# Optimization experiments

Measured on AMD Instinct MI355X. Metric: run time of the kernel, lower is better.

The kernel has to match this reference:

```python
import jax, jax.numpy as jnp
import numpy as np

B, S, E = 2, 2048, 1024
H, KV, D = 16, 4, 64
GC = 128          # ve_gate_channels
EPS = 1.1920929e-07  # torch F.rms_norm default eps for fp32
NEG = -1e30


def setup_inputs() -> dict:
    key = jax.random.key(0)
    ks = jax.random.split(key, 8)
    x = jax.random.normal(ks[0], (B, S, E), jnp.float32)
    ve = jax.random.normal(ks[1], (B, S, KV * D), jnp.float32)
    half = D // 2
    inv_freq = 1.0 / (10000.0 ** (np.arange(half, dtype=np.float64) / half))
    ang = np.arange(S, dtype=np.float64)[:, None] * inv_freq[None, :]
    cos = jnp.asarray(np.cos(ang), jnp.float32)[:, None, :]  # [S,1,D/2]
    sin = jnp.asarray(np.sin(ang), jnp.float32)[:, None, :]
    sc = E ** -0.5
    Wq = jax.random.normal(ks[2], (E, H * D), jnp.float32) * sc
    Wk = jax.random.normal(ks[3], (E, KV * D), jnp.float32) * sc
    Wv = jax.random.normal(ks[4], (E, KV * D), jnp.float32) * sc
    Wproj = jax.random.normal(ks[5], (E, E), jnp.float32) * sc
    Wgate = jax.random.normal(ks[6], (GC, KV), jnp.float32) * (GC ** -0.5)
    return {"x": x, "ve": ve, "cos": cos, "sin": sin, "Wq": Wq, "Wk": Wk,
            "Wv": Wv, "Wproj": Wproj, "Wgate": Wgate,
            "window_left": 1024, "window_right": 0}


def _rms(x):
    return x * jax.lax.rsqrt(jnp.mean(x * x, axis=-1, keepdims=True) + EPS)


def _rope(x, cos, sin):
    d = x.shape[-1] // 2
    x1, x2 = x[..., :d], x[..., d:]
    return jnp.concatenate([x1 * cos + x2 * sin, -x1 * sin + x2 * cos], axis=-1)


def reference(x, ve, cos, sin, Wq, Wk, Wv, Wproj, Wgate, window_left, window_right):
    b, s, e = x.shape
    q = (x @ Wq).reshape(b, s, H, D)
    k = (x @ Wk).reshape(b, s, KV, D)
    v = (x @ Wv).reshape(b, s, KV, D)
    # value-embedding gate: 2*sigmoid over first GC channels, per kv-head
    gate = 2.0 * jax.nn.sigmoid(x[..., :GC] @ Wgate)          # [B,S,KV]
    v = v + gate[..., None] * ve.reshape(b, s, KV, D)
    q = _rms(_rope(q, cos, sin))
    k = _rms(_rope(k, cos, sin))
    # GQA: repeat kv heads to match query heads
    g = H // KV
    kk = jnp.repeat(k, g, axis=2)                             # [B,S,H,D]
    vv = jnp.repeat(v, g, axis=2)
    scores = jnp.einsum('bihd,bjhd->bhij', q, kk) * (D ** -0.5)
    i = jnp.arange(s)[:, None]
    j = jnp.arange(s)[None, :]
    mask = (j <= i + window_right) & (j >= i - window_left) & (j <= i)
    scores = jnp.where(mask, scores, NEG)
    p = jax.nn.softmax(scores, axis=-1)
    y = jnp.einsum('bhij,bjhd->bihd', p, vv).reshape(b, s, H * D)
    return y @ Wproj
```

## Files before the change

### kernel.cpp

```cpp
#include <hip/hip_runtime.h>

typedef __bf16 bf16;
typedef __bf16 bf16x4 __attribute__((ext_vector_type(4)));
typedef __bf16 bf16x8 __attribute__((ext_vector_type(8)));
typedef float floatx4 __attribute__((ext_vector_type(4)));

#define EPS 1.1920929e-07f
#define QSCALE (0.125f * 1.44269504088896f)
#define SHIFT_C 11.5416f

__device__ __forceinline__ floatx4 mfma16(bf16x8 a, bf16x8 b, floatx4 c) {
  return __builtin_amdgcn_mfma_f32_16x16x32_bf16(a, b, c, 0, 0, 0);
}

__device__ __forceinline__ void gload16(const void* g, void* l) {
  __builtin_amdgcn_global_load_lds((const __attribute__((address_space(1))) unsigned int*)g,
                                   (__attribute__((address_space(3))) unsigned int*)l, 16, 0, 0);
}

__global__ void cast_x_kernel(const float* __restrict__ x, bf16* __restrict__ xb) {
  int i = (blockIdx.x * blockDim.x + threadIdx.x) * 4;
  float4 v = *(const float4*)(x + i);
  bf16x4 o = {(bf16)v.x, (bf16)v.y, (bf16)v.z, (bf16)v.w};
  *(bf16x4*)(xb + i) = o;
}

__global__ void pack_wqkv_kernel(const float* __restrict__ Wq, const float* __restrict__ Wk,
                                 const float* __restrict__ Wv, bf16* __restrict__ out) {
  __shared__ float tile[32][33];
  int n0 = blockIdx.x * 32, k0 = blockIdx.y * 32;
  int tx = threadIdx.x & 31, ty = threadIdx.x >> 5;
#pragma unroll
  for (int i = 0; i < 4; i++) {
    int k = k0 + ty + i * 8, n = n0 + tx;
    float v;
    if (n < 1024)      v = Wq[(size_t)k * 1024 + n];
    else if (n < 1280) v = Wk[(size_t)k * 256 + (n - 1024)];
    else               v = Wv[(size_t)k * 256 + (n - 1280)];
    tile[ty + i * 8][tx] = v;
  }
  __syncthreads();
#pragma unroll
  for (int i = 0; i < 4; i++) {
    int n = n0 + ty + i * 8, k = k0 + tx;
    out[(size_t)n * 1024 + k] = (bf16)tile[tx][ty + i * 8];
  }
}

__global__ void trans_wproj_kernel(const float* __restrict__ W, bf16* __restrict__ out) {
  __shared__ float tile[32][33];
  int n0 = blockIdx.x * 32, k0 = blockIdx.y * 32;
  int tx = threadIdx.x & 31, ty = threadIdx.x >> 5;
#pragma unroll
  for (int i = 0; i < 4; i++)
    tile[ty + i * 8][tx] = W[(size_t)(k0 + ty + i * 8) * 1024 + n0 + tx];
  __syncthreads();
#pragma unroll
  for (int i = 0; i < 4; i++)
    out[(size_t)(n0 + ty + i * 8) * 1024 + k0 + tx] = (bf16)tile[tx][ty + i * 8];
}

template <bool OUT_BF16>
__global__ __launch_bounds__(256) void gemm_kernel(const bf16* __restrict__ A,
                                                   const bf16* __restrict__ Bt,
                                                   void* __restrict__ Cout,
                                                   int M, int N, int K) {
  __shared__ bf16 As[128 * 32];
  __shared__ bf16 Bs[64 * 32];
  const int tid = threadIdx.x;
  const int m0 = blockIdx.y * 128, n0 = blockIdx.x * 64;
  const int w = tid >> 6, lane = tid & 63;
  const int q = lane >> 4, r0 = lane & 15;
  const int wm = w & 1, wn = w >> 1;
  const int lrow = lane >> 2, lcol = (lane & 3) * 8;

  floatx4 acc[4][2];
#pragma unroll
  for (int i = 0; i < 4; i++)
#pragma unroll
    for (int j = 0; j < 2; j++) acc[i][j] = (floatx4){0.f, 0.f, 0.f, 0.f};

  for (int k0 = 0; k0 < K; k0 += 32) {
    __syncthreads();
    gload16(A + (size_t)(m0 + w * 16 + lrow) * K + k0 + lcol, &As[(w * 16) * 32]);
    gload16(A + (size_t)(m0 + 64 + w * 16 + lrow) * K + k0 + lcol, &As[(64 + w * 16) * 32]);
    gload16(Bt + (size_t)(n0 + w * 16 + lrow) * K + k0 + lcol, &Bs[(w * 16) * 32]);
    __syncthreads();
    bf16x8 af[4], bfr[2];
#pragma unroll
    for (int mt = 0; mt < 4; mt++) af[mt] = *(const bf16x8*)&As[(wm * 64 + mt * 16 + r0) * 32 + q * 8];
#pragma unroll
    for (int nt = 0; nt < 2; nt++) bfr[nt] = *(const bf16x8*)&Bs[(wn * 32 + nt * 16 + r0) * 32 + q * 8];
#pragma unroll
    for (int mt = 0; mt < 4; mt++)
#pragma unroll
      for (int nt = 0; nt < 2; nt++)
        acc[mt][nt] = mfma16(af[mt], bfr[nt], acc[mt][nt]);
  }
#pragma unroll
  for (int mt = 0; mt < 4; mt++)
#pragma unroll
    for (int nt = 0; nt < 2; nt++)
#pragma unroll
      for (int r = 0; r < 4; r++) {
        int row = m0 + wm * 64 + mt * 16 + q * 4 + r;
        int col = n0 + wn * 32 + nt * 16 + r0;
        float v = acc[mt][nt][r];
        if (OUT_BF16) ((bf16*)Cout)[(size_t)row * N + col] = (bf16)v;
        else          ((float*)Cout)[(size_t)row * N + col] = v;
      }
}

__global__ void postproc_kernel(const bf16* __restrict__ qkv, const float* __restrict__ x,
                                const float* __restrict__ ve, const float* __restrict__ cosb,
                                const float* __restrict__ sinb, const float* __restrict__ wgate,
                                bf16* __restrict__ Qb, bf16* __restrict__ Kb, bf16* __restrict__ Vb) {
  int t = blockIdx.x;
  int b = t >> 11, s = t & 2047;
  int w = threadIdx.x >> 6, lane = threadIdx.x & 63;

  const float* xrow = x + (size_t)t * 1024;
  float g = xrow[lane] * wgate[lane * 4 + w] + xrow[64 + lane] * wgate[(64 + lane) * 4 + w];
  for (int m = 1; m < 64; m <<= 1) g += __shfl_xor(g, m, 64);
  g = 2.f / (1.f + __expf(-g));

  int d = lane & 31;
  float c = cosb[s * 32 + d], sn = sinb[s * 32 + d];
  float sgn = (lane < 32) ? sn : -sn;
  const bf16* qrow = qkv + (size_t)t * 1536;

#pragma unroll
  for (int i = 0; i < 4; i++) {
    int h = w * 4 + i;
    float v = (float)qrow[h * 64 + lane];
    float p = __shfl_xor(v, 32, 64);
    float rv = v * c + p * sgn;
    float ss = rv * rv;
    for (int m = 1; m < 64; m <<= 1) ss += __shfl_xor(ss, m, 64);
    float outq = rv * rsqrtf(ss * (1.f / 64.f) + EPS) * QSCALE;
    Qb[(((size_t)b * 16 + h) * 2048 + s) * 64 + lane] = (bf16)outq;
  }
  {
    float v = (float)qrow[1024 + w * 64 + lane];
    float p = __shfl_xor(v, 32, 64);
    float rv = v * c + p * sgn;
    float ss = rv * rv;
    for (int m = 1; m < 64; m <<= 1) ss += __shfl_xor(ss, m, 64);
    float outk = rv * rsqrtf(ss * (1.f / 64.f) + EPS);
    Kb[(((size_t)b * 4 + w) * 2048 + s) * 64 + lane] = (bf16)outk;
    float vv = (float)qrow[1280 + w * 64 + lane] + g * ve[(size_t)t * 256 + w * 64 + lane];
    Vb[(((size_t)b * 4 + w) * 2048 + s) * 64 + lane] = (bf16)vv;
  }
}

__global__ void pack_kv_kernel(const bf16* __restrict__ Kb, const bf16* __restrict__ Vb,
                               bf16* __restrict__ Kf, bf16* __restrict__ Vf) {
  __shared__ bf16 Ks[64 * 72];
  __shared__ bf16 Vs[64 * 72];
  int chunk = blockIdx.x;
  int bkv = blockIdx.y;
  const bf16* kin = Kb + ((size_t)bkv * 2048 + chunk * 64) * 64;
  const bf16* vin = Vb + ((size_t)bkv * 2048 + chunk * 64) * 64;
  int t = threadIdx.x;
  int row = t >> 3, col = (t & 7) * 8;
#pragma unroll
  for (int i = 0; i < 2; i++) {
    *(uint4*)&Ks[(row + 32 * i) * 72 + col] = *(const uint4*)(kin + (size_t)(row + 32 * i) * 64 + col);
    *(uint4*)&Vs[(row + 32 * i) * 72 + col] = *(const uint4*)(vin + (size_t)(row + 32 * i) * 64 + col);
  }
  __syncthreads();
  int lane = t & 63, q = (t >> 4) & 3, r0 = t & 15;
  int sub = t >> 7;
  int pair = (t >> 6) & 1;
  size_t tbase = ((size_t)bkv * 64 + chunk * 2 + sub) * 2048;
#pragma unroll
  for (int i = 0; i < 2; i++) {
    int w = pair * 2 + i;
    int jl = sub * 32 + (w >= 2 ? 16 : 0) + r0;
    int d0 = (w & 1) * 32 + q * 8;
    *(uint4*)&Kf[tbase + w * 512 + lane * 8] = *(const uint4*)&Ks[jl * 72 + d0];
  }
#pragma unroll
  for (int i = 0; i < 2; i++) {
    int nt = pair * 2 + i;
    int d = nt * 16 + r0;
    bf16 tmp[8];
#pragma unroll
    for (int e = 0; e < 8; e++) {
      int jl = sub * 32 + (e >> 2) * 16 + 4 * q + (e & 3);
      tmp[e] = Vs[jl * 72 + d];
    }
    *(uint4*)&Vf[tbase + nt * 512 + lane * 8] = *(uint4*)tmp;
  }
}

__global__ __launch_bounds__(512, 4) void attn_kernel(const bf16* __restrict__ Qb,
                                                      const bf16* __restrict__ Kf,
                                                      const bf16* __restrict__ Vf,
                                                      const int* __restrict__ wlp,
                                                      const int* __restrict__ wrp,
                                                      bf16* __restrict__ Yb) {
  __shared__ float Ol[4 * 64 * 21];
  const int wl = wlp[0];
  const int wrc = min(wrp[0], 0);
  const int blk = blockIdx.x;
  const int qc = 31 - (blk & 31);
  const int bh = blk >> 5;
  const int b = bh >> 4, h = bh & 15, kvh = (bh & 15) >> 2;
  const int w = threadIdx.x >> 6, lane = threadIdx.x & 63;
  const int wq = w & 3, jh = w >> 2;
  const int q = lane >> 4, r0 = lane & 15;
  const int q0 = qc * 64 + wq * 16;

  const bf16* qbase = Qb + (((size_t)b * 16 + h) * 2048 + q0 + r0) * 64;
  bf16x8 aq0 = *(const bf16x8*)(qbase + q * 8);
  bf16x8 aq1 = *(const bf16x8*)(qbase + 32 + q * 8);

  floatx4 Oacc[4];
#pragma unroll
  for (int nt = 0; nt < 4; nt++) Oacc[nt] = (floatx4){0.f, 0.f, 0.f, 0.f};
  floatx4 Lacc = (floatx4){0.f, 0.f, 0.f, 0.f};

  const bf16 onev = (bf16)1.0f;
  const bf16x8 ones = {onev, onev, onev, onev, onev, onev, onev, onev};

  const int jlo0 = max(0, q0 - wl) & ~31;
  const int jhi = q0 + 15 + wrc;
  const int n = ((jhi - jlo0) >> 5) + 1;
  const int nlo = (n + 1) >> 1;
  const int jstart = jh ? jlo0 + (nlo << 5) : jlo0;
  const int count = jh ? n - nlo : nlo;

  const bf16* kfb = Kf + ((size_t)(b * 4 + kvh) * 64) * 2048 + lane * 8;
  const bf16* vfb = Vf + ((size_t)(b * 4 + kvh) * 64) * 2048 + lane * 8;

  if (count > 0) {
    int tile0 = jstart >> 5;
    bf16x8 kf[4], vf[4], nk[4], nv[4];
#pragma unroll
    for (int u = 0; u < 4; u++) {
      kf[u] = *(const bf16x8*)(kfb + (size_t)tile0 * 2048 + u * 512);
      vf[u] = *(const bf16x8*)(vfb + (size_t)tile0 * 2048 + u * 512);
    }

    for (int t = 0; t < count; t++) {
      const int j0 = jstart + (t << 5);
      const int tn = (t + 1 < count) ? tile0 + t + 1 : tile0 + t;
#pragma unroll
      for (int u = 0; u < 4; u++) {
        nk[u] = *(const bf16x8*)(kfb + (size_t)tn * 2048 + u * 512);
        nv[u] = *(const bf16x8*)(vfb + (size_t)tn * 2048 + u * 512);
      }

      floatx4 s0 = (floatx4){-SHIFT_C, -SHIFT_C, -SHIFT_C, -SHIFT_C};
      floatx4 s1 = s0;
      s0 = mfma16(kf[0], aq0, s0);
      s0 = mfma16(kf[1], aq1, s0);
      s1 = mfma16(kf[2], aq0, s1);
      s1 = mfma16(kf[3], aq1, s1);

      bf16x8 pa;
      if (j0 >= q0 + 15 - wl && j0 + 31 <= q0 + wrc) {
#pragma unroll
        for (int r = 0; r < 4; r++) {
          pa[r] = (bf16)exp2f(s0[r]);
          pa[4 + r] = (bf16)exp2f(s1[r]);
        }
      } else {
        const int i = q0 + r0;
#pragma unroll
        for (int r = 0; r < 4; r++) {
          int ja = j0 + 4 * q + r, jb = ja + 16;
          bool va = (ja <= i + wrc) && (ja >= i - wl);
          bool vb = (jb <= i + wrc) && (jb >= i - wl);
          pa[r] = va ? (bf16)exp2f(s0[r]) : (bf16)0.f;
          pa[4 + r] = vb ? (bf16)exp2f(s1[r]) : (bf16)0.f;
        }
      }

      Lacc = mfma16(pa, ones, Lacc);
#pragma unroll
      for (int nt = 0; nt < 4; nt++) Oacc[nt] = mfma16(pa, vf[nt], Oacc[nt]);

#pragma unroll
      for (int u = 0; u < 4; u++) { kf[u] = nk[u]; vf[u] = nv[u]; }
    }
  }

  float* mbase = Ol + (wq * 64 + lane) * 21;
  if (jh == 1) {
#pragma unroll
    for (int nt = 0; nt < 4; nt++)
#pragma unroll
      for (int r = 0; r < 4; r++) mbase[nt * 4 + r] = Oacc[nt][r];
#pragma unroll
    for (int r = 0; r < 4; r++) mbase[16 + r] = Lacc[r];
  }
  __syncthreads();
  if (jh == 0) {
    float inv[4];
#pragma unroll
    for (int r = 0; r < 4; r++) inv[r] = 1.f / (Lacc[r] + mbase[16 + r]);
#pragma unroll
    for (int nt = 0; nt < 4; nt++)
#pragma unroll
      for (int r = 0; r < 4; r++) {
        int i = q0 + q * 4 + r;
        float o = (Oacc[nt][r] + mbase[nt * 4 + r]) * inv[r];
        Yb[((size_t)b * 2048 + i) * 1024 + h * 64 + nt * 16 + r0] = (bf16)o;
      }
  }
}

extern "C" void kernel_launch(void* const* d_in, const int* in_sizes, int n_in,
                              void* d_out, int out_size, void* d_ws, size_t ws_size,
                              hipStream_t stream) {
  const float* x     = (const float*)d_in[0];
  const float* ve    = (const float*)d_in[1];
  const float* cosb  = (const float*)d_in[2];
  const float* sinb  = (const float*)d_in[3];
  const float* Wq    = (const float*)d_in[4];
  const float* Wk    = (const float*)d_in[5];
  const float* Wv    = (const float*)d_in[6];
  const float* Wproj = (const float*)d_in[7];
  const float* Wgate = (const float*)d_in[8];
  const int* wl      = (const int*)d_in[9];
  const int* wr      = (const int*)d_in[10];

  char* ws = (char*)d_ws;
  bf16* Xb      = (bf16*)(ws);
  bf16* Wqkv_t  = (bf16*)(ws + 8388608);
  bf16* Wproj_t = (bf16*)(ws + 11534336);
  bf16* qkvb    = (bf16*)(ws + 13631488);
  bf16* Qb      = (bf16*)(ws + 26214400);
  bf16* Kb      = (bf16*)(ws + 34603008);
  bf16* Kf      = (bf16*)(ws + 36700160);
  bf16* Yb      = (bf16*)(ws + 38797312);
  bf16* Vb      = Yb;
  bf16* Vf      = qkvb;

  cast_x_kernel<<<4096, 256, 0, stream>>>(x, Xb);
  pack_wqkv_kernel<<<dim3(48, 32), 256, 0, stream>>>(Wq, Wk, Wv, Wqkv_t);
  trans_wproj_kernel<<<dim3(32, 32), 256, 0, stream>>>(Wproj, Wproj_t);
  gemm_kernel<true><<<dim3(24, 32), 256, 0, stream>>>(Xb, Wqkv_t, qkvb, 4096, 1536, 1024);
  postproc_kernel<<<4096, 256, 0, stream>>>(qkvb, x, ve, cosb, sinb, Wgate, Qb, Kb, Vb);
  pack_kv_kernel<<<dim3(32, 8), 256, 0, stream>>>(Kb, Vb, Kf, Vf);
  attn_kernel<<<1024, 512, 0, stream>>>(Qb, Kf, Vf, wl, wr, Yb);
  gemm_kernel<false><<<dim3(16, 32), 256, 0, stream>>>(Yb, Wproj_t, d_out, 4096, 1024, 1024);
}
```

Before: 198.4 us.

## Fuse RoPE, RMS norm, value gate and KV packing into QKV GEMM epilogue

The QKV GEMM now uses 128x128 tiles, and its epilogue does the work of the old postproc and pack kernels. It applies RoPE and RMS norm to Q and K, adds the gated value embedding to V, and writes Q, K and V straight into the attention-ready layouts through LDS staging. This removes the bf16 qkv intermediate round trip and two launches. A small separate kernel computes the sigmoid gate. The output projection GEMM also moves to 128x128 tiles. The trade-off is fewer blocks per GEMM (384 and 256), which may lower occupancy and load balance on a 256-CU device, plus the new serial gate kernel.

```diff
diff --git a/kernel.cpp b/kernel.cpp
--- a/kernel.cpp
+++ b/kernel.cpp
@@ -60,138 +60,240 @@
     out[(size_t)(n0 + ty + i * 8) * 1024 + k0 + tx] = (bf16)tile[tx][ty + i * 8];
 }
 
-template <bool OUT_BF16>
-__global__ __launch_bounds__(256) void gemm_kernel(const bf16* __restrict__ A,
-                                                   const bf16* __restrict__ Bt,
-                                                   void* __restrict__ Cout,
-                                                   int M, int N, int K) {
-  __shared__ bf16 As[128 * 32];
-  __shared__ bf16 Bs[64 * 32];
+__global__ void gate_kernel(const float* __restrict__ x, const float* __restrict__ wgate,
+                            float* __restrict__ gate) {
+  int tid = blockIdx.x * 256 + threadIdx.x;
+  int t = tid >> 2, kv = tid & 3;
+  const float* xr = x + (size_t)t * 1024;
+  float g = 0.f;
+#pragma unroll 4
+  for (int c = 0; c < 128; c++) g += xr[c] * wgate[c * 4 + kv];
+  int b = t >> 11, s = t & 2047;
+  gate[((size_t)b * 4 + kv) * 2048 + s] = 2.f / (1.f + __expf(-g));
+}
+
+__global__ __launch_bounds__(256) void qkv_gemm_kernel(const bf16* __restrict__ A,
+                                                       const bf16* __restrict__ Bt,
+                                                       const float* __restrict__ ve,
+                                                       const float* __restrict__ cosb,
+                                                       const float* __restrict__ sinb,
+                                                       const float* __restrict__ gate,
+                                                       bf16* __restrict__ Qb,
+                                                       bf16* __restrict__ Kf,
+                                                       bf16* __restrict__ Vf) {
+  __shared__ __align__(16) char smem[36864];
+  bf16* As = (bf16*)smem;
+  bf16* Bs = (bf16*)(smem + 8192);
+  bf16* Ep = (bf16*)smem;
+  const int K = 1024;
   const int tid = threadIdx.x;
-  const int m0 = blockIdx.y * 128, n0 = blockIdx.x * 64;
+  const int tile = blockIdx.x;
+  const int m0 = blockIdx.y * 128, n0 = tile * 128;
   const int w = tid >> 6, lane = tid & 63;
   const int q = lane >> 4, r0 = lane & 15;
   const int wm = w & 1, wn = w >> 1;
   const int lrow = lane >> 2, lcol = (lane & 3) * 8;
-
-  floatx4 acc[4][2];
+  const int b = m0 >> 11, s0 = m0 & 2047;
+
+  floatx4 acc[4][4];
 #pragma unroll
   for (int i = 0; i < 4; i++)
 #pragma unroll
-    for (int j = 0; j < 2; j++) acc[i][j] = (floatx4){0.f, 0.f, 0.f, 0.f};
+    for (int j = 0; j < 4; j++) acc[i][j] = (floatx4){0.f, 0.f, 0.f, 0.f};
 
   for (int k0 = 0; k0 < K; k0 += 32) {
     __syncthreads();
-    gload16(A + (size_t)(m0 + w * 16 + lrow) * K + k0 + lcol, &As[(w * 16) * 32]);
-    gload16(A + (size_t)(m0 + 64 + w * 16 + lrow) * K + k0 + lcol, &As[(64 + w * 16) * 32]);
-    gload16(Bt + (size_t)(n0 + w * 16 + lrow) * K + k0 + lcol, &Bs[(w * 16) * 32]);
-    __syncthreads();
-    bf16x8 af[4], bfr[2];
+    gload16(A + (size_t)(m0 + w * 32 + lrow) * K + k0 + lcol, &As[(w * 32) * 32]);
+    gload16(A + (size_t)(m0 + w * 32 + 16 + lrow) * K + k0 + lcol, &As[(w * 32 + 16) * 32]);
+    gload16(Bt + (size_t)(n0 + w * 32 + lrow) * K + k0 + lcol, &Bs[(w * 32) * 32]);
+    gload16(Bt + (size_t)(n0 + w * 32 + 16 + lrow) * K + k0 + lcol, &Bs[(w * 32 + 16) * 32]);
+    __syncthreads();
+    bf16x8 af[4], bfr[4];
 #pragma unroll
     for (int mt = 0; mt < 4; mt++) af[mt] = *(const bf16x8*)&As[(wm * 64 + mt * 16 + r0) * 32 + q * 8];
 #pragma unroll
-    for (int nt = 0; nt < 2; nt++) bfr[nt] = *(const bf16x8*)&Bs[(wn * 32 + nt * 16 + r0) * 32 + q * 8];
+    for (int nt = 0; nt < 4; nt++) bfr[nt] = *(const bf16x8*)&Bs[(wn * 64 + nt * 16 + r0) * 32 + q * 8];
 #pragma unroll
     for (int mt = 0; mt < 4; mt++)
 #pragma unroll
-      for (int nt = 0; nt < 2; nt++)
+      for (int nt = 0; nt < 4; nt++)
         acc[mt][nt] = mfma16(af[mt], bfr[nt], acc[mt][nt]);
   }
+  __syncthreads();
+
+  if (tile < 8) {
+#pragma unroll
+    for (int mt = 0; mt < 4; mt++) {
+      float rvv[4][4];
+#pragma unroll
+      for (int ntp = 0; ntp < 2; ntp++) {
+        int d31 = ntp * 16 + r0;
+#pragma unroll
+        for (int r = 0; r < 4; r++) {
+          int s = s0 + wm * 64 + mt * 16 + q * 4 + r;
+          float c = cosb[s * 32 + d31], sn = sinb[s * 32 + d31];
+          float v1 = acc[mt][ntp][r], v2 = acc[mt][ntp + 2][r];
+          rvv[ntp][r] = v1 * c + v2 * sn;
+          rvv[ntp + 2][r] = v2 * c - v1 * sn;
+        }
+      }
+#pragma unroll
+      for (int r = 0; r < 4; r++) {
+        float ss = 0.f;
+#pragma unroll
+        for (int nt = 0; nt < 4; nt++) ss += rvv[nt][r] * rvv[nt][r];
+        ss += __shfl_xor(ss, 1, 64);
+        ss += __shfl_xor(ss, 2, 64);
+        ss += __shfl_xor(ss, 4, 64);
+        ss += __shfl_xor(ss, 8, 64);
+        float sc = rsqrtf(ss * (1.f / 64.f) + EPS) * QSCALE;
+        int row = wm * 64 + mt * 16 + q * 4 + r;
+#pragma unroll
+        for (int nt = 0; nt < 4; nt++)
+          Ep[(wn * 128 + row) * 72 + nt * 16 + r0] = (bf16)(rvv[nt][r] * sc);
+      }
+    }
+    __syncthreads();
+#pragma unroll
+    for (int p = 0; p < 8; p++) {
+      int g = p * 256 + tid;
+      int plane = g >> 10, rem = g & 1023, row = rem >> 3, chunk = rem & 7;
+      uint4 val = *(const uint4*)&Ep[(plane * 128 + row) * 72 + chunk * 8];
+      int h = tile * 2 + plane;
+      *(uint4*)&Qb[(((size_t)b * 16 + h) * 2048 + s0 + row) * 64 + chunk * 8] = val;
+    }
+  } else if (tile < 10) {
+    int kv = (tile - 8) * 2 + wn;
+#pragma unroll
+    for (int mt = 0; mt < 4; mt++) {
+      float rvv[4][4];
+#pragma unroll
+      for (int ntp = 0; ntp < 2; ntp++) {
+        int d31 = ntp * 16 + r0;
+#pragma unroll
+        for (int r = 0; r < 4; r++) {
+          int s = s0 + wm * 64 + mt * 16 + q * 4 + r;
+          float c = cosb[s * 32 + d31], sn = sinb[s * 32 + d31];
+          float v1 = acc[mt][ntp][r], v2 = acc[mt][ntp + 2][r];
+          rvv[ntp][r] = v1 * c + v2 * sn;
+          rvv[ntp + 2][r] = v2 * c - v1 * sn;
+        }
+      }
+#pragma unroll
+      for (int r = 0; r < 4; r++) {
+        float ss = 0.f;
+#pragma unroll
+        for (int nt = 0; nt < 4; nt++) ss += rvv[nt][r] * rvv[nt][r];
+        ss += __shfl_xor(ss, 1, 64);
+        ss += __shfl_xor(ss, 2, 64);
+        ss += __shfl_xor(ss, 4, 64);
+        ss += __shfl_xor(ss, 8, 64);
+        float sc = rsqrtf(ss * (1.f / 64.f) + EPS);
+        int row = wm * 64 + mt * 16 + q * 4 + r;
+#pragma unroll
+        for (int nt = 0; nt < 4; nt++)
+          Ep[(wn * 128 + row) * 72 + nt * 16 + r0] = (bf16)(rvv[nt][r] * sc);
+      }
+    }
+    __syncthreads();
+#pragma unroll
+    for (int st = 0; st < 2; st++) {
+      int tk = (s0 >> 5) + wm * 2 + st;
+      size_t tb = ((size_t)(b * 4 + kv) * 64 + tk) * 2048;
+#pragma unroll
+      for (int u = 0; u < 4; u++) {
+        int joff = (u >= 2) ? 16 : 0, doff = (u & 1) * 32;
+        bf16x8 f = *(const bf16x8*)&Ep[(wn * 128 + wm * 64 + st * 32 + joff + r0) * 72 + doff + q * 8];
+        *(bf16x8*)&Kf[tb + u * 512 + lane * 8] = f;
+      }
+    }
+  } else {
+    int kv = (tile - 10) * 2 + wn;
+    const float* gbase = gate + ((size_t)b * 4 + kv) * 2048;
+#pragma unroll
+    for (int mt = 0; mt < 4; mt++) {
+#pragma unroll
+      for (int r = 0; r < 4; r++) {
+        int row = wm * 64 + mt * 16 + q * 4 + r;
+        int t = m0 + row;
+        float gg = gbase[s0 + row];
+#pragma unroll
+        for (int nt = 0; nt < 4; nt++) {
+          int d = nt * 16 + r0;
+          float vv = acc[mt][nt][r] + gg * ve[(size_t)t * 256 + kv * 64 + d];
+          Ep[(wn * 128 + row) * 72 + d] = (bf16)vv;
+        }
+      }
+    }
+    __syncthreads();
+#pragma unroll
+    for (int st = 0; st < 2; st++) {
+      int tk = (s0 >> 5) + wm * 2 + st;
+      size_t tb = ((size_t)(b * 4 + kv) * 64 + tk) * 2048;
+#pragma unroll
+      for (int nt = 0; nt < 4; nt++) {
+        bf16 tmp[8];
+#pragma unroll
+        for (int e = 0; e < 8; e++) {
+          int jl = wm * 64 + st * 32 + (e >> 2) * 16 + 4 * q + (e & 3);
+          tmp[e] = Ep[(wn * 128 + jl) * 72 + nt * 16 + r0];
+        }
+        *(uint4*)&Vf[tb + nt * 512 + lane * 8] = *(uint4*)tmp;
+      }
+    }
+  }
+}
+
+template <bool OUT_BF16>
+__global__ __launch_bounds__(256) void gemm128_kernel(const bf16* __restrict__ A,
+                                                      const bf16* __restrict__ Bt,
+                                                      void* __restrict__ Cout,
+                                                      int M, int N, int K) {
+  __shared__ __align__(16) bf16 As[128 * 32];
+  __shared__ __align__(16) bf16 Bs[128 * 32];
+  const int tid = threadIdx.x;
+  const int m0 = blockIdx.y * 128, n0 = blockIdx.x * 128;
+  const int w = tid >> 6, lane = tid & 63;
+  const int q = lane >> 4, r0 = lane & 15;
+  const int wm = w & 1, wn = w >> 1;
+  const int lrow = lane >> 2, lcol = (lane & 3) * 8;
+
+  floatx4 acc[4][4];
+#pragma unroll
+  for (int i = 0; i < 4; i++)
+#pragma unroll
+    for (int j = 0; j < 4; j++) acc[i][j] = (floatx4){0.f, 0.f, 0.f, 0.f};
+
+  for (int k0 = 0; k0 < K; k0 += 32) {
+    __syncthreads();
+    gload16(A + (size_t)(m0 + w * 32 + lrow) * K + k0 + lcol, &As[(w * 32) * 32]);
+    gload16(A + (size_t)(m0 + w * 32 + 16 + lrow) * K + k0 + lcol, &As[(w * 32 + 16) * 32]);
+    gload16(Bt + (size_t)(n0 + w * 32 + lrow) * K + k0 + lcol, &Bs[(w * 32) * 32]);
+    gload16(Bt + (size_t)(n0 + w * 32 + 16 + lrow) * K + k0 + lcol, &Bs[(w * 32 + 16) * 32]);
+    __syncthreads();
+    bf16x8 af[4], bfr[4];
+#pragma unroll
+    for (int mt = 0; mt < 4; mt++) af[mt] = *(const bf16x8*)&As[(wm * 64 + mt * 16 + r0) * 32 + q * 8];
+#pragma unroll
+    for (int nt = 0; nt < 4; nt++) bfr[nt] = *(const bf16x8*)&Bs[(wn * 64 + nt * 16 + r0) * 32 + q * 8];
+#pragma unroll
+    for (int mt = 0; mt < 4; mt++)
+#pragma unroll
+      for (int nt = 0; nt < 4; nt++)
+        acc[mt][nt] = mfma16(af[mt], bfr[nt], acc[mt][nt]);
+  }
 #pragma unroll
   for (int mt = 0; mt < 4; mt++)
 #pragma unroll
-    for (int nt = 0; nt < 2; nt++)
+    for (int nt = 0; nt < 4; nt++)
 #pragma unroll
       for (int r = 0; r < 4; r++) {
         int row = m0 + wm * 64 + mt * 16 + q * 4 + r;
-        int col = n0 + wn * 32 + nt * 16 + r0;
+        int col = n0 + wn * 64 + nt * 16 + r0;
         float v = acc[mt][nt][r];
         if (OUT_BF16) ((bf16*)Cout)[(size_t)row * N + col] = (bf16)v;
         else          ((float*)Cout)[(size_t)row * N + col] = v;
       }
-}
-
-__global__ void postproc_kernel(const bf16* __restrict__ qkv, const float* __restrict__ x,
-                                const float* __restrict__ ve, const float* __restrict__ cosb,
-                                const float* __restrict__ sinb, const float* __restrict__ wgate,
-                                bf16* __restrict__ Qb, bf16* __restrict__ Kb, bf16* __restrict__ Vb) {
-  int t = blockIdx.x;
-  int b = t >> 11, s = t & 2047;
-  int w = threadIdx.x >> 6, lane = threadIdx.x & 63;
-
-  const float* xrow = x + (size_t)t * 1024;
-  float g = xrow[lane] * wgate[lane * 4 + w] + xrow[64 + lane] * wgate[(64 + lane) * 4 + w];
-  for (int m = 1; m < 64; m <<= 1) g += __shfl_xor(g, m, 64);
-  g = 2.f / (1.f + __expf(-g));
-
-  int d = lane & 31;
-  float c = cosb[s * 32 + d], sn = sinb[s * 32 + d];
-  float sgn = (lane < 32) ? sn : -sn;
-  const bf16* qrow = qkv + (size_t)t * 1536;
-
-#pragma unroll
-  for (int i = 0; i < 4; i++) {
-    int h = w * 4 + i;
-    float v = (float)qrow[h * 64 + lane];
-    float p = __shfl_xor(v, 32, 64);
-    float rv = v * c + p * sgn;
-    float ss = rv * rv;
-    for (int m = 1; m < 64; m <<= 1) ss += __shfl_xor(ss, m, 64);
-    float outq = rv * rsqrtf(ss * (1.f / 64.f) + EPS) * QSCALE;
-    Qb[(((size_t)b * 16 + h) * 2048 + s) * 64 + lane] = (bf16)outq;
-  }
-  {
-    float v = (float)qrow[1024 + w * 64 + lane];
-    float p = __shfl_xor(v, 32, 64);
-    float rv = v * c + p * sgn;
-    float ss = rv * rv;
-    for (int m = 1; m < 64; m <<= 1) ss += __shfl_xor(ss, m, 64);
-    float outk = rv * rsqrtf(ss * (1.f / 64.f) + EPS);
-    Kb[(((size_t)b * 4 + w) * 2048 + s) * 64 + lane] = (bf16)outk;
-    float vv = (float)qrow[1280 + w * 64 + lane] + g * ve[(size_t)t * 256 + w * 64 + lane];
-    Vb[(((size_t)b * 4 + w) * 2048 + s) * 64 + lane] = (bf16)vv;
-  }
-}
-
-__global__ void pack_kv_kernel(const bf16* __restrict__ Kb, const bf16* __restrict__ Vb,
-                               bf16* __restrict__ Kf, bf16* __restrict__ Vf) {
-  __shared__ bf16 Ks[64 * 72];
-  __shared__ bf16 Vs[64 * 72];
-  int chunk = blockIdx.x;
-  int bkv = blockIdx.y;
-  const bf16* kin = Kb + ((size_t)bkv * 2048 + chunk * 64) * 64;
-  const bf16* vin = Vb + ((size_t)bkv * 2048 + chunk * 64) * 64;
-  int t = threadIdx.x;
-  int row = t >> 3, col = (t & 7) * 8;
-#pragma unroll
-  for (int i = 0; i < 2; i++) {
-    *(uint4*)&Ks[(row + 32 * i) * 72 + col] = *(const uint4*)(kin + (size_t)(row + 32 * i) * 64 + col);
-    *(uint4*)&Vs[(row + 32 * i) * 72 + col] = *(const uint4*)(vin + (size_t)(row + 32 * i) * 64 + col);
-  }
-  __syncthreads();
-  int lane = t & 63, q = (t >> 4) & 3, r0 = t & 15;
-  int sub = t >> 7;
-  int pair = (t >> 6) & 1;
-  size_t tbase = ((size_t)bkv * 64 + chunk * 2 + sub) * 2048;
-#pragma unroll
-  for (int i = 0; i < 2; i++) {
-    int w = pair * 2 + i;
-    int jl = sub * 32 + (w >= 2 ? 16 : 0) + r0;
-    int d0 = (w & 1) * 32 + q * 8;
-    *(uint4*)&Kf[tbase + w * 512 + lane * 8] = *(const uint4*)&Ks[jl * 72 + d0];
-  }
-#pragma unroll
-  for (int i = 0; i < 2; i++) {
-    int nt = pair * 2 + i;
-    int d = nt * 16 + r0;
-    bf16 tmp[8];
-#pragma unroll
-    for (int e = 0; e < 8; e++) {
-      int jl = sub * 32 + (e >> 2) * 16 + 4 * q + (e & 3);
-      tmp[e] = Vs[jl * 72 + d];
-    }
-    *(uint4*)&Vf[tbase + nt * 512 + lane * 8] = *(uint4*)tmp;
-  }
 }
 
 __global__ __launch_bounds__(512, 4) void attn_kernel(const bf16* __restrict__ Qb,
@@ -331,20 +433,17 @@
   bf16* Xb      = (bf16*)(ws);
   bf16* Wqkv_t  = (bf16*)(ws + 8388608);
   bf16* Wproj_t = (bf16*)(ws + 11534336);
-  bf16* qkvb    = (bf16*)(ws + 13631488);
-  bf16* Qb      = (bf16*)(ws + 26214400);
-  bf16* Kb      = (bf16*)(ws + 34603008);
-  bf16* Kf      = (bf16*)(ws + 36700160);
-  bf16* Yb      = (bf16*)(ws + 38797312);
-  bf16* Vb      = Yb;
-  bf16* Vf      = qkvb;
+  bf16* Qb      = (bf16*)(ws + 13631488);
+  bf16* Kf      = (bf16*)(ws + 22020096);
+  bf16* Vf      = (bf16*)(ws + 24117248);
+  bf16* Yb      = (bf16*)(ws + 26214400);
+  float* gateb  = (float*)(ws + 34603008);
 
   cast_x_kernel<<<4096, 256, 0, stream>>>(x, Xb);
   pack_wqkv_kernel<<<dim3(48, 32), 256, 0, stream>>>(Wq, Wk, Wv, Wqkv_t);
   trans_wproj_kernel<<<dim3(32, 32), 256, 0, stream>>>(Wproj, Wproj_t);
-  gemm_kernel<true><<<dim3(24, 32), 256, 0, stream>>>(Xb, Wqkv_t, qkvb, 4096, 1536, 1024);
-  postproc_kernel<<<4096, 256, 0, stream>>>(qkvb, x, ve, cosb, sinb, Wgate, Qb, Kb, Vb);
-  pack_kv_kernel<<<dim3(32, 8), 256, 0, stream>>>(Kb, Vb, Kf, Vf);
+  gate_kernel<<<64, 256, 0, stream>>>(x, Wgate, gateb);
+  qkv_gemm_kernel<<<dim3(12, 32), 256, 0, stream>>>(Xb, Wqkv_t, ve, cosb, sinb, gateb, Qb, Kf, Vf);
   attn_kernel<<<1024, 512, 0, stream>>>(Qb, Kf, Vf, wl, wr, Yb);
-  gemm_kernel<false><<<dim3(16, 32), 256, 0, stream>>>(Yb, Wproj_t, d_out, 4096, 1024, 1024);
-}
+  gemm128_kernel<false><<<dim3(8, 32), 256, 0, stream>>>(Yb, Wproj_t, d_out, 4096, 1024, 1024);
+}
```

New measurement: 200.7 us. No clear change (+1.1%).
